# Performance work log

Hardware: AMD Instinct MI355X
Metric: run time of the kernel (lower is better)

## Reference

```python
import jax, jax.numpy as jnp
import numpy as np

N_TP = 4  # number of heterogeneous agent types (experts)


def _mlp(x, w1, b1, w2, b2, w3, b3):
    h = jax.nn.relu(x @ w1 + b1)
    h = jax.nn.relu(h @ w2 + b2)
    return h @ w3 + b3


def setup_inputs() -> dict:
    key = jax.random.key(0)
    ks = jax.random.split(key, 12)
    T, A, D, H, NA = 2048, 128, 64, 64, 16
    s = 0.05
    return {
        "obs": jax.random.normal(ks[0], (T, A, D), dtype=jnp.float32),
        "hete_pick": jax.random.randint(ks[1], (T, A), 0, N_TP, dtype=jnp.int64),
        "gp_sel_summary": jax.random.uniform(ks[2], (T, N_TP), dtype=jnp.float32),
        "W1": jax.random.normal(ks[3], (N_TP, D + N_TP, H), dtype=jnp.float32) * s,
        "b1": jnp.zeros((N_TP, H), jnp.float32),
        "W2": jax.random.normal(ks[4], (N_TP, H, H), dtype=jnp.float32) * s,
        "b2": jnp.zeros((N_TP, H), jnp.float32),
        "W3": jax.random.normal(ks[5], (N_TP, H, NA), dtype=jnp.float32) * s,
        "b3": jnp.zeros((N_TP, NA), jnp.float32),
        "cW1": jax.random.normal(ks[6], (D + N_TP, H), dtype=jnp.float32) * s,
        "cb1": jnp.zeros((H,), jnp.float32),
        "cW2": jax.random.normal(ks[7], (H, H), dtype=jnp.float32) * s,
        "cb2": jnp.zeros((H,), jnp.float32),
        "cW3": jax.random.normal(ks[8], (H, 1), dtype=jnp.float32) * s,
        "cb3": jnp.zeros((1,), jnp.float32),
    }


def reference(obs, hete_pick, gp_sel_summary, W1, b1, W2, b2, W3, b3,
              cW1, cb1, cW2, cb2, cW3, cb3):
    T, A, D = obs.shape
    n_tp = W1.shape[0]
    # hete_info_obs: broadcast group-selection summary over agents, concat to obs
    hete_info = jnp.broadcast_to(gp_sel_summary[:, None, :], (T, A, n_tp))
    x = jnp.concatenate([obs, hete_info.astype(obs.dtype)], axis=-1)  # [T,A,D+n_tp]
    xf = x.reshape(T * A, D + n_tp)
    tp = hete_pick.reshape(T * A)
    # per-type dispatch: mask -> sub-net -> scatter back (expressed as masked select)
    logits = jnp.zeros((T * A, W3.shape[-1]), obs.dtype)
    for t in range(n_tp):
        out_t = _mlp(xf, W1[t], b1[t], W2[t], b2[t], W3[t], b3[t])
        logits = jnp.where((tp == t)[:, None], out_t, logits)
    # central critic runs on all agents
    value = _mlp(xf, cW1, cb1, cW2, cb2, cW3, cb3)  # [T*A,1]
    out = jnp.concatenate([logits, value], axis=-1)  # [T*A, n_action+1]
    return out.reshape(T, A, -1)
```

## Files before the change

kernel.cpp:

```cpp
#include <hip/hip_runtime.h>
#include <stdint.h>


typedef float v4f __attribute__((ext_vector_type(4)));
typedef short v8s __attribute__((ext_vector_type(8)));

#define XS_STR 104
#define HS_STR 136
#define WP2_OFF 30720
#define WP3_OFF 51200

static __device__ __forceinline__ short f2bf(float f) {
    union { float f; uint32_t u; } c; c.f = f;
    uint32_t u = c.u;
    uint32_t r = (u + 0x7FFFu + ((u >> 16) & 1u)) >> 16;
    return (short)r;
}


__global__ void count_kernel(const int* __restrict__ hete, int* __restrict__ cnt) {
    __shared__ int wc[4][4];
    int tid = threadIdx.x, lane = tid & 63, w = tid >> 6;
    int base = blockIdx.x * 1024;
    int lc[4] = {0, 0, 0, 0};
#pragma unroll
    for (int c = 0; c < 4; c++) {
        int e = hete[base + c * 256 + tid];
#pragma unroll
        for (int t = 0; t < 4; t++) {
            unsigned long long m = __ballot(e == t);
            if (lane == 0) lc[t] += __popcll(m);
        }
    }
    if (lane == 0)
#pragma unroll
        for (int t = 0; t < 4; t++) wc[w][t] = lc[t];
    __syncthreads();
    if (tid < 4)
        cnt[blockIdx.x * 4 + tid] = wc[0][tid] + wc[1][tid] + wc[2][tid] + wc[3][tid];
}

__global__ void prefix_kernel(const int* __restrict__ cnt, int* __restrict__ hdr,
                              int* __restrict__ bb, int* __restrict__ bucket) {
    __shared__ int s[4][256];
    __shared__ int sa[5], sC[4];
    int tid = threadIdx.x;
    int c0[4];
#pragma unroll
    for (int t = 0; t < 4; t++) { c0[t] = cnt[tid * 4 + t]; s[t][tid] = c0[t]; }
    __syncthreads();
    for (int off = 1; off < 256; off <<= 1) {
        int v[4];
#pragma unroll
        for (int t = 0; t < 4; t++) v[t] = (tid >= off) ? s[t][tid - off] : 0;
        __syncthreads();
#pragma unroll
        for (int t = 0; t < 4; t++) s[t][tid] += v[t];
        __syncthreads();
    }
    if (tid == 0) {
        int a = 0, ts = 0;
        for (int e = 0; e < 4; e++) {
            int c = s[e][255];
            sC[e] = c;
            sa[e] = a;
            hdr[8 + e]  = a;
            hdr[13 + e] = ts;
            int tiles = (c + 127) >> 7;
            a  += tiles << 7;
            ts += tiles;
        }
        sa[4]   = a;
        hdr[12] = a;
        hdr[17] = ts;
    }
    __syncthreads();
#pragma unroll
    for (int t = 0; t < 4; t++) bb[tid * 4 + t] = sa[t] + s[t][tid] - c0[t];
    for (int e = 0; e < 4; e++) {
        int start = sa[e] + sC[e], end = sa[e + 1];
        for (int i = start + tid; i < end; i += 256) bucket[i] = -1;
    }
}

__global__ void scatter_kernel(const int* __restrict__ hete, const int* __restrict__ bb,
                               int* __restrict__ bucket) {
    __shared__ int cur[4];
    int tid = threadIdx.x, lane = tid & 63;
    if (tid < 4) cur[tid] = bb[blockIdx.x * 4 + tid];
    __syncthreads();
    unsigned long long lt = (1ull << lane) - 1ull;
#pragma unroll
    for (int c = 0; c < 4; c++) {
        int i = blockIdx.x * 1024 + c * 256 + tid;
        int e = hete[i];
        int slot = 0;
#pragma unroll
        for (int t = 0; t < 4; t++) {
            unsigned long long m = __ballot(e == t);
            int n = __popcll(m);
            int wb = 0;
            if (lane == 0 && n) wb = atomicAdd(&cur[t], n);
            wb = __shfl(wb, 0);
            if (e == t) slot = wb + __popcll(m & lt);
        }
        bucket[slot] = i;
    }
}

__global__ void prep_kernel(const float* __restrict__ W1, const float* __restrict__ cW1,
                            const float* __restrict__ W2, const float* __restrict__ cW2,
                            const float* __restrict__ W3, const float* __restrict__ cW3,
                            short* __restrict__ wp) {
    int b = blockIdx.x, lane = threadIdx.x;
    int nl = lane & 15, quad = lane >> 4;
    short frag[8];
    if (b < 60) {
        int e = b / 12, rem = b % 12, ks = rem / 4, nt = rem % 4;
        int n = nt * 16 + nl;
#pragma unroll
        for (int j = 0; j < 8; j++) {
            int k = ks * 32 + quad * 8 + j;
            float v = 0.f;
            if (k < 68) v = (e < 4) ? W1[(e * 68 + k) * 64 + n] : cW1[k * 64 + n];
            frag[j] = f2bf(v);
        }
    } else if (b < 100) {
        int u = b - 60, e = u / 8, ks = (u % 8) / 4, nt = u % 4;
        int n = nt * 16 + nl;
#pragma unroll
        for (int j = 0; j < 8; j++) {
            int k = ks * 32 + quad * 8 + j;
            frag[j] = f2bf((e < 4) ? W2[(e * 64 + k) * 64 + n] : cW2[k * 64 + n]);
        }
    } else {
        int u = b - 100;
#pragma unroll
        for (int j = 0; j < 8; j++) {
            int ks = (u < 8) ? (u & 1) : (u - 8);
            int k  = ks * 32 + quad * 8 + j;
            float v;
            if (u < 8) { int ee = u >> 1; v = W3[(ee * 64 + k) * 16 + nl]; }
            else       { v = (nl == 0) ? cW3[k] : 0.f; }
            frag[j] = f2bf(v);
        }
    }
    v8s pk = { frag[0], frag[1], frag[2], frag[3], frag[4], frag[5], frag[6], frag[7] };
    *(v8s*)(wp + (size_t)b * 512 + lane * 8) = pk;
}


__global__ __launch_bounds__(256) void main_kernel(
    const float* __restrict__ obs, const float* __restrict__ gp,
    const int* __restrict__ bucket, const int* __restrict__ hdr,
    const short* __restrict__ wp,
    const float* __restrict__ b1, const float* __restrict__ b2, const float* __restrict__ b3,
    const float* __restrict__ cb1, const float* __restrict__ cb2, const float* __restrict__ cb3,
    float* __restrict__ out)
{
    __shared__ __align__(16) short buf[128 * HS_STR];
    __shared__ int tokL[128];
    short* xs = buf;
    short* hs = buf;

    int b = blockIdx.x;
    int total = hdr[17];
    if (b >= total) return;
    int e = 3;
    if      (b < hdr[14]) e = 0;
    else if (b < hdr[15]) e = 1;
    else if (b < hdr[16]) e = 2;
    int slot0 = hdr[8 + e] + (b - hdr[13 + e]) * 128;

    int tid = threadIdx.x, lane = tid & 63, w = tid >> 6;
    int ml = lane & 15, quad = lane >> 4;

    if (tid < 128) tokL[tid] = bucket[slot0 + tid];

    {
        int r = tid >> 1, hh = tid & 1;
        int tk = bucket[slot0 + r];
        v8s z = { 0, 0, 0, 0, 0, 0, 0, 0 };
        if (tk >= 0) {
            const float4* src = (const float4*)(obs + (size_t)tk * 64 + hh * 32);
#pragma unroll
            for (int t = 0; t < 4; t++) {
                float4 f0 = src[2 * t], f1 = src[2 * t + 1];
                v8s pk = { f2bf(f0.x), f2bf(f0.y), f2bf(f0.z), f2bf(f0.w),
                           f2bf(f1.x), f2bf(f1.y), f2bf(f1.z), f2bf(f1.w) };
                *(v8s*)&xs[r * XS_STR + hh * 32 + t * 8] = pk;
            }
            if (hh) {
                const float* g = gp + (size_t)(tk >> 7) * 4;
                v8s pg = { f2bf(g[0]), f2bf(g[1]), f2bf(g[2]), f2bf(g[3]), 0, 0, 0, 0 };
                *(v8s*)&xs[r * XS_STR + 64] = pg;
                *(v8s*)&xs[r * XS_STR + 72] = z;
                *(v8s*)&xs[r * XS_STR + 80] = z;
                *(v8s*)&xs[r * XS_STR + 88] = z;
            }
        } else {
#pragma unroll
            for (int t = 0; t < 4; t++) *(v8s*)&xs[r * XS_STR + hh * 32 + t * 8] = z;
            if (hh) {
                *(v8s*)&xs[r * XS_STR + 64] = z;
                *(v8s*)&xs[r * XS_STR + 72] = z;
                *(v8s*)&xs[r * XS_STR + 80] = z;
                *(v8s*)&xs[r * XS_STR + 88] = z;
            }
        }
    }
    __syncthreads();

    v4f accE[8], accC[8];
#pragma unroll
    for (int m = 0; m < 8; m++) { accE[m] = (v4f){0,0,0,0}; accC[m] = (v4f){0,0,0,0}; }
#pragma unroll
    for (int ks = 0; ks < 3; ks++) {
        v8s bE = *(const v8s*)(wp + (size_t)((e * 3 + ks) * 4 + w) * 512 + lane * 8);
        v8s bC = *(const v8s*)(wp + (size_t)((12 + ks) * 4 + w) * 512 + lane * 8);
#pragma unroll
        for (int m = 0; m < 8; m++) {
            v8s a = *(const v8s*)&xs[(m * 16 + ml) * XS_STR + ks * 32 + quad * 8];
            accE[m] = __builtin_amdgcn_mfma_f32_16x16x32_bf16(a, bE, accE[m], 0, 0, 0);
            accC[m] = __builtin_amdgcn_mfma_f32_16x16x32_bf16(a, bC, accC[m], 0, 0, 0);
        }
    }
    __syncthreads();
    {
        float bE1 = b1[e * 64 + w * 16 + ml], bC1 = cb1[w * 16 + ml];
#pragma unroll
        for (int m = 0; m < 8; m++)
#pragma unroll
            for (int rr = 0; rr < 4; rr++) {
                int row = m * 16 + quad * 4 + rr;
                hs[row * HS_STR + w * 16 + ml]      = f2bf(fmaxf(accE[m][rr] + bE1, 0.f));
                hs[row * HS_STR + 64 + w * 16 + ml] = f2bf(fmaxf(accC[m][rr] + bC1, 0.f));
            }
    }
    __syncthreads();

    v4f acc2E[8], acc2C[8];
#pragma unroll
    for (int m = 0; m < 8; m++) { acc2E[m] = (v4f){0,0,0,0}; acc2C[m] = (v4f){0,0,0,0}; }
#pragma unroll
    for (int ks = 0; ks < 2; ks++) {
        v8s bE = *(const v8s*)(wp + WP2_OFF + (size_t)((e * 2 + ks) * 4 + w) * 512 + lane * 8);
        v8s bC = *(const v8s*)(wp + WP2_OFF + (size_t)((8 + ks) * 4 + w) * 512 + lane * 8);
#pragma unroll
        for (int m = 0; m < 8; m++) {
            v8s aE = *(const v8s*)&hs[(m * 16 + ml) * HS_STR + ks * 32 + quad * 8];
            v8s aC = *(const v8s*)&hs[(m * 16 + ml) * HS_STR + 64 + ks * 32 + quad * 8];
            acc2E[m] = __builtin_amdgcn_mfma_f32_16x16x32_bf16(aE, bE, acc2E[m], 0, 0, 0);
            acc2C[m] = __builtin_amdgcn_mfma_f32_16x16x32_bf16(aC, bC, acc2C[m], 0, 0, 0);
        }
    }
    __syncthreads();
    {
        float bE2 = b2[e * 64 + w * 16 + ml], bC2 = cb2[w * 16 + ml];
#pragma unroll
        for (int m = 0; m < 8; m++)
#pragma unroll
            for (int rr = 0; rr < 4; rr++) {
                int row = m * 16 + quad * 4 + rr;
                hs[row * HS_STR + w * 16 + ml]      = f2bf(fmaxf(acc2E[m][rr] + bE2, 0.f));
                hs[row * HS_STR + 64 + w * 16 + ml] = f2bf(fmaxf(acc2C[m][rr] + bC2, 0.f));
            }
    }
    __syncthreads();

    v4f accL[2], accV[2];
#pragma unroll
    for (int mm = 0; mm < 2; mm++) { accL[mm] = (v4f){0,0,0,0}; accV[mm] = (v4f){0,0,0,0}; }
#pragma unroll
    for (int ks = 0; ks < 2; ks++) {
        v8s bW = *(const v8s*)(wp + WP3_OFF + (size_t)(e * 2 + ks) * 512 + lane * 8);
        v8s bV = *(const v8s*)(wp + WP3_OFF + (size_t)(8 + ks) * 512 + lane * 8);
#pragma unroll
        for (int mm = 0; mm < 2; mm++) {
            v8s aE = *(const v8s*)&hs[((2 * w + mm) * 16 + ml) * HS_STR + ks * 32 + quad * 8];
            v8s aC = *(const v8s*)&hs[((2 * w + mm) * 16 + ml) * HS_STR + 64 + ks * 32 + quad * 8];
            accL[mm] = __builtin_amdgcn_mfma_f32_16x16x32_bf16(aE, bW, accL[mm], 0, 0, 0);
            accV[mm] = __builtin_amdgcn_mfma_f32_16x16x32_bf16(aC, bV, accV[mm], 0, 0, 0);
        }
    }

    {
        float b3v = b3[e * 16 + ml], cb3v = cb3[0];
#pragma unroll
        for (int mm = 0; mm < 2; mm++)
#pragma unroll
            for (int rr = 0; rr < 4; rr++) {
                int row = (2 * w + mm) * 16 + quad * 4 + rr;
                int tk = tokL[row];
                if (tk >= 0) {
                    float* o = out + (size_t)tk * 17;
                    o[ml] = accL[mm][rr] + b3v;
                    if (ml == 0) o[16] = accV[mm][rr] + cb3v;
                }
            }
    }
}


extern "C" void kernel_launch(void* const* d_in, const int* in_sizes, int n_in,
                              void* d_out, int out_size, void* d_ws, size_t ws_size,
                              hipStream_t stream) {
    const float* obs = (const float*)d_in[0];
    const int*  hete = (const int*)d_in[1];
    const float* gp  = (const float*)d_in[2];
    const float* W1  = (const float*)d_in[3];
    const float* b1  = (const float*)d_in[4];
    const float* W2  = (const float*)d_in[5];
    const float* b2  = (const float*)d_in[6];
    const float* W3  = (const float*)d_in[7];
    const float* b3  = (const float*)d_in[8];
    const float* cW1 = (const float*)d_in[9];
    const float* cb1 = (const float*)d_in[10];
    const float* cW2 = (const float*)d_in[11];
    const float* cb2 = (const float*)d_in[12];
    const float* cW3 = (const float*)d_in[13];
    const float* cb3 = (const float*)d_in[14];
    float* out = (float*)d_out;

    int*   hdr    = (int*)d_ws;
    int*   bucket = hdr + 32;
    int*   cnt    = bucket + 262656;
    int*   bb     = cnt + 1024;
    short* wp     = (short*)(bb + 1024);

    count_kernel  <<<256, 256, 0, stream>>>(hete, cnt);
    prefix_kernel <<<1,   256, 0, stream>>>(cnt, hdr, bb, bucket);
    scatter_kernel<<<256, 256, 0, stream>>>(hete, bb, bucket);
    prep_kernel   <<<110,  64, 0, stream>>>(W1, cW1, W2, cW2, W3, cW3, wp);
    main_kernel   <<<2051, 256, 0, stream>>>(obs, gp, bucket, hdr, wp,
                                             b1, b2, b3, cb1, cb2, cb3, out);
}
```

Baseline: 157.8 us.

## Replace global bucket sort with per-block local expert grouping

Removes the count, prefix and scatter kernels and instead has each block take 128 contiguous tokens, sort them by expert type in shared memory via ballots, and pad each expert group to 16-row tiles (up to 11 tiles). Per-tile expert weights are selected through a packed expert map. This drops three kernel launches and the gathered obs reads through a global bucket array, at the cost of padding waste (up to 176 rows instead of 128), per-tile weight loads, and larger register and shared-memory use. It also adds launch_bounds occupancy hint 3.

```diff
diff --git a/kernel.cpp b/kernel.cpp
--- a/kernel.cpp
+++ b/kernel.cpp
@@ -7,105 +7,19 @@
 
 #define XS_STR 104
 #define HS_STR 136
+#define MAXR   176
+#define MAXT   11
 #define WP2_OFF 30720
 #define WP3_OFF 51200
+
+#define SEL4(te, a0, a1, a2, a3) \
+    ((te) < 2 ? ((te) == 0 ? (a0) : (a1)) : ((te) == 2 ? (a2) : (a3)))
 
 static __device__ __forceinline__ short f2bf(float f) {
     union { float f; uint32_t u; } c; c.f = f;
     uint32_t u = c.u;
     uint32_t r = (u + 0x7FFFu + ((u >> 16) & 1u)) >> 16;
     return (short)r;
-}
-
-
-__global__ void count_kernel(const int* __restrict__ hete, int* __restrict__ cnt) {
-    __shared__ int wc[4][4];
-    int tid = threadIdx.x, lane = tid & 63, w = tid >> 6;
-    int base = blockIdx.x * 1024;
-    int lc[4] = {0, 0, 0, 0};
-#pragma unroll
-    for (int c = 0; c < 4; c++) {
-        int e = hete[base + c * 256 + tid];
-#pragma unroll
-        for (int t = 0; t < 4; t++) {
-            unsigned long long m = __ballot(e == t);
-            if (lane == 0) lc[t] += __popcll(m);
-        }
-    }
-    if (lane == 0)
-#pragma unroll
-        for (int t = 0; t < 4; t++) wc[w][t] = lc[t];
-    __syncthreads();
-    if (tid < 4)
-        cnt[blockIdx.x * 4 + tid] = wc[0][tid] + wc[1][tid] + wc[2][tid] + wc[3][tid];
-}
-
-__global__ void prefix_kernel(const int* __restrict__ cnt, int* __restrict__ hdr,
-                              int* __restrict__ bb, int* __restrict__ bucket) {
-    __shared__ int s[4][256];
-    __shared__ int sa[5], sC[4];
-    int tid = threadIdx.x;
-    int c0[4];
-#pragma unroll
-    for (int t = 0; t < 4; t++) { c0[t] = cnt[tid * 4 + t]; s[t][tid] = c0[t]; }
-    __syncthreads();
-    for (int off = 1; off < 256; off <<= 1) {
-        int v[4];
-#pragma unroll
-        for (int t = 0; t < 4; t++) v[t] = (tid >= off) ? s[t][tid - off] : 0;
-        __syncthreads();
-#pragma unroll
-        for (int t = 0; t < 4; t++) s[t][tid] += v[t];
-        __syncthreads();
-    }
-    if (tid == 0) {
-        int a = 0, ts = 0;
-        for (int e = 0; e < 4; e++) {
-            int c = s[e][255];
-            sC[e] = c;
-            sa[e] = a;
-            hdr[8 + e]  = a;
-            hdr[13 + e] = ts;
-            int tiles = (c + 127) >> 7;
-            a  += tiles << 7;
-            ts += tiles;
-        }
-        sa[4]   = a;
-        hdr[12] = a;
-        hdr[17] = ts;
-    }
-    __syncthreads();
-#pragma unroll
-    for (int t = 0; t < 4; t++) bb[tid * 4 + t] = sa[t] + s[t][tid] - c0[t];
-    for (int e = 0; e < 4; e++) {
-        int start = sa[e] + sC[e], end = sa[e + 1];
-        for (int i = start + tid; i < end; i += 256) bucket[i] = -1;
-    }
-}
-
-__global__ void scatter_kernel(const int* __restrict__ hete, const int* __restrict__ bb,
-                               int* __restrict__ bucket) {
-    __shared__ int cur[4];
-    int tid = threadIdx.x, lane = tid & 63;
-    if (tid < 4) cur[tid] = bb[blockIdx.x * 4 + tid];
-    __syncthreads();
-    unsigned long long lt = (1ull << lane) - 1ull;
-#pragma unroll
-    for (int c = 0; c < 4; c++) {
-        int i = blockIdx.x * 1024 + c * 256 + tid;
-        int e = hete[i];
-        int slot = 0;
-#pragma unroll
-        for (int t = 0; t < 4; t++) {
-            unsigned long long m = __ballot(e == t);
-            int n = __popcll(m);
-            int wb = 0;
-            if (lane == 0 && n) wb = atomicAdd(&cur[t], n);
-            wb = __shfl(wb, 0);
-            if (e == t) slot = wb + __popcll(m & lt);
-        }
-        bucket[slot] = i;
-    }
 }
 
 __global__ void prep_kernel(const float* __restrict__ W1, const float* __restrict__ cW1,
@@ -150,154 +64,245 @@
 }
 
 
-__global__ __launch_bounds__(256) void main_kernel(
-    const float* __restrict__ obs, const float* __restrict__ gp,
-    const int* __restrict__ bucket, const int* __restrict__ hdr,
-    const short* __restrict__ wp,
+__global__ __launch_bounds__(256, 3) void main_kernel(
+    const float* __restrict__ obs, const int* __restrict__ hete,
+    const float* __restrict__ gp, const short* __restrict__ wp,
     const float* __restrict__ b1, const float* __restrict__ b2, const float* __restrict__ b3,
     const float* __restrict__ cb1, const float* __restrict__ cb2, const float* __restrict__ cb3,
     float* __restrict__ out)
 {
-    __shared__ __align__(16) short buf[128 * HS_STR];
-    __shared__ int tokL[128];
+    __shared__ __align__(16) short buf[MAXR * HS_STR];
+    __shared__ int rowtok[MAXR];
+    __shared__ int tslot[128];
+    __shared__ int wcnt[2][4];
+
     short* xs = buf;
     short* hs = buf;
 
-    int b = blockIdx.x;
-    int total = hdr[17];
-    if (b >= total) return;
-    int e = 3;
-    if      (b < hdr[14]) e = 0;
-    else if (b < hdr[15]) e = 1;
-    else if (b < hdr[16]) e = 2;
-    int slot0 = hdr[8 + e] + (b - hdr[13 + e]) * 128;
-
-    int tid = threadIdx.x, lane = tid & 63, w = tid >> 6;
-    int ml = lane & 15, quad = lane >> 4;
-
-    if (tid < 128) tokL[tid] = bucket[slot0 + tid];
+    const int b = blockIdx.x;
+    const int tid = threadIdx.x, lane = tid & 63, w = tid >> 6;
+    const int ml = lane & 15, quad = lane >> 4;
+    const int col = w * 16 + ml;
+    const size_t base = (size_t)b * 128;
+
+    const int ltk = tid >> 1, hh = tid & 1;
+    const float4* src = (const float4*)(obs + (base + ltk) * 64 + hh * 32);
+    float4 f[8];
+#pragma unroll
+    for (int t = 0; t < 8; t++) f[t] = src[t];
+
+    const float* gpb = gp + (size_t)b * 4;
+    float g0 = gpb[0], g1 = gpb[1], g2 = gpb[2], g3 = gpb[3];
+
+    if (tid < MAXR) rowtok[tid] = -1;
+
+    int e = 0, rank = 0;
+    if (tid < 128) {
+        e = hete[base + tid];
+        unsigned long long ltm = (1ull << lane) - 1ull;
+        unsigned long long m0 = __ballot(e == 0);
+        unsigned long long m1 = __ballot(e == 1);
+        unsigned long long m2 = __ballot(e == 2);
+        unsigned long long m3 = __ballot(e == 3);
+        if      (e == 0) rank = __popcll(m0 & ltm);
+        else if (e == 1) rank = __popcll(m1 & ltm);
+        else if (e == 2) rank = __popcll(m2 & ltm);
+        else             rank = __popcll(m3 & ltm);
+        if (lane == 0) {
+            wcnt[w][0] = __popcll(m0); wcnt[w][1] = __popcll(m1);
+            wcnt[w][2] = __popcll(m2); wcnt[w][3] = __popcll(m3);
+        }
+    }
+    __syncthreads();
+
+    int c0 = wcnt[0][0] + wcnt[1][0];
+    int c1 = wcnt[0][1] + wcnt[1][1];
+    int c2 = wcnt[0][2] + wcnt[1][2];
+    int c3 = wcnt[0][3] + wcnt[1][3];
+    int p0 = (c0 + 15) & ~15, p1 = (c1 + 15) & ~15;
+    int p2 = (c2 + 15) & ~15, p3 = (c3 + 15) & ~15;
+    int gs1 = p0, gs2 = p0 + p1, gs3 = p0 + p1 + p2;
+    int padded = gs3 + p3;
+    int ntiles = padded >> 4;
+    int n1 = p1 >> 4, n2 = p2 >> 4, n3 = p3 >> 4;
+    int t1 = gs1 >> 4, t2 = gs2 >> 4, t3 = gs3 >> 4;
+    int epack = ((0x55555555 & ((1 << (2 * n1)) - 1)) * 1) << (2 * t1)
+              | ((0x55555555 & ((1 << (2 * n2)) - 1)) * 2) << (2 * t2)
+              | ((0x55555555 & ((1 << (2 * n3)) - 1)) * 3) << (2 * t3);
+
+    if (tid < 128) {
+        int gsE  = SEL4(e, 0, gs1, gs2, gs3);
+        int woff = (w == 1) ? wcnt[0][e] : 0;
+        int slot = gsE + woff + rank;
+        rowtok[slot] = tid;
+        tslot[tid]   = slot;
+    }
+    __syncthreads();
 
     {
-        int r = tid >> 1, hh = tid & 1;
-        int tk = bucket[slot0 + r];
         v8s z = { 0, 0, 0, 0, 0, 0, 0, 0 };
-        if (tk >= 0) {
-            const float4* src = (const float4*)(obs + (size_t)tk * 64 + hh * 32);
-#pragma unroll
-            for (int t = 0; t < 4; t++) {
-                float4 f0 = src[2 * t], f1 = src[2 * t + 1];
-                v8s pk = { f2bf(f0.x), f2bf(f0.y), f2bf(f0.z), f2bf(f0.w),
-                           f2bf(f1.x), f2bf(f1.y), f2bf(f1.z), f2bf(f1.w) };
-                *(v8s*)&xs[r * XS_STR + hh * 32 + t * 8] = pk;
-            }
-            if (hh) {
-                const float* g = gp + (size_t)(tk >> 7) * 4;
-                v8s pg = { f2bf(g[0]), f2bf(g[1]), f2bf(g[2]), f2bf(g[3]), 0, 0, 0, 0 };
-                *(v8s*)&xs[r * XS_STR + 64] = pg;
-                *(v8s*)&xs[r * XS_STR + 72] = z;
-                *(v8s*)&xs[r * XS_STR + 80] = z;
-                *(v8s*)&xs[r * XS_STR + 88] = z;
-            }
-        } else {
-#pragma unroll
-            for (int t = 0; t < 4; t++) *(v8s*)&xs[r * XS_STR + hh * 32 + t * 8] = z;
-            if (hh) {
-                *(v8s*)&xs[r * XS_STR + 64] = z;
-                *(v8s*)&xs[r * XS_STR + 72] = z;
-                *(v8s*)&xs[r * XS_STR + 80] = z;
-                *(v8s*)&xs[r * XS_STR + 88] = z;
-            }
-        }
-    }
-    __syncthreads();
-
-    v4f accE[8], accC[8];
-#pragma unroll
-    for (int m = 0; m < 8; m++) { accE[m] = (v4f){0,0,0,0}; accC[m] = (v4f){0,0,0,0}; }
+        int s = tslot[ltk];
+        int rb = s * XS_STR + hh * 32;
+#pragma unroll
+        for (int t = 0; t < 4; t++) {
+            float4 a0 = f[2 * t], a1 = f[2 * t + 1];
+            v8s pk = { f2bf(a0.x), f2bf(a0.y), f2bf(a0.z), f2bf(a0.w),
+                       f2bf(a1.x), f2bf(a1.y), f2bf(a1.z), f2bf(a1.w) };
+            *(v8s*)&xs[rb + t * 8] = pk;
+        }
+        if (hh) {
+            v8s pg = { f2bf(g0), f2bf(g1), f2bf(g2), f2bf(g3), 0, 0, 0, 0 };
+            *(v8s*)&xs[s * XS_STR + 64] = pg;
+            *(v8s*)&xs[s * XS_STR + 72] = z;
+            *(v8s*)&xs[s * XS_STR + 80] = z;
+            *(v8s*)&xs[s * XS_STR + 88] = z;
+        }
+#pragma unroll
+        for (int p = 0; p < 2; p++) {
+            int r = p * 128 + ltk;
+            if (r < padded && rowtok[r] < 0) {
+#pragma unroll
+                for (int t = 0; t < 4; t++) *(v8s*)&xs[r * XS_STR + hh * 32 + t * 8] = z;
+                if (hh) {
+                    *(v8s*)&xs[r * XS_STR + 64] = z;
+                    *(v8s*)&xs[r * XS_STR + 72] = z;
+                    *(v8s*)&xs[r * XS_STR + 80] = z;
+                    *(v8s*)&xs[r * XS_STR + 88] = z;
+                }
+            }
+        }
+    }
+    __syncthreads();
+
+    v4f accE[MAXT], accC[MAXT];
+#pragma unroll
+    for (int mt = 0; mt < MAXT; mt++) { accE[mt] = (v4f){0,0,0,0}; accC[mt] = (v4f){0,0,0,0}; }
+
+    v8s bC1f[3];
+#pragma unroll
+    for (int ks = 0; ks < 3; ks++)
+        bC1f[ks] = *(const v8s*)(wp + (size_t)((12 + ks) * 4 + w) * 512 + lane * 8);
+
 #pragma unroll
     for (int ks = 0; ks < 3; ks++) {
-        v8s bE = *(const v8s*)(wp + (size_t)((e * 3 + ks) * 4 + w) * 512 + lane * 8);
-        v8s bC = *(const v8s*)(wp + (size_t)((12 + ks) * 4 + w) * 512 + lane * 8);
-#pragma unroll
-        for (int m = 0; m < 8; m++) {
-            v8s a = *(const v8s*)&xs[(m * 16 + ml) * XS_STR + ks * 32 + quad * 8];
-            accE[m] = __builtin_amdgcn_mfma_f32_16x16x32_bf16(a, bE, accE[m], 0, 0, 0);
-            accC[m] = __builtin_amdgcn_mfma_f32_16x16x32_bf16(a, bC, accC[m], 0, 0, 0);
-        }
-    }
-    __syncthreads();
+#pragma unroll
+        for (int mt = 0; mt < MAXT; mt++) {
+            if (mt < ntiles) {
+                int te = (epack >> (2 * mt)) & 3;
+                v8s bE = *(const v8s*)(wp + (size_t)((te * 3 + ks) * 4 + w) * 512 + lane * 8);
+                v8s a  = *(const v8s*)&xs[(mt * 16 + ml) * XS_STR + ks * 32 + quad * 8];
+                accE[mt] = __builtin_amdgcn_mfma_f32_16x16x32_bf16(a, bE,       accE[mt], 0, 0, 0);
+                accC[mt] = __builtin_amdgcn_mfma_f32_16x16x32_bf16(a, bC1f[ks], accC[mt], 0, 0, 0);
+            }
+        }
+    }
+    __syncthreads();
+
     {
-        float bE1 = b1[e * 64 + w * 16 + ml], bC1 = cb1[w * 16 + ml];
-#pragma unroll
-        for (int m = 0; m < 8; m++)
-#pragma unroll
-            for (int rr = 0; rr < 4; rr++) {
-                int row = m * 16 + quad * 4 + rr;
-                hs[row * HS_STR + w * 16 + ml]      = f2bf(fmaxf(accE[m][rr] + bE1, 0.f));
-                hs[row * HS_STR + 64 + w * 16 + ml] = f2bf(fmaxf(accC[m][rr] + bC1, 0.f));
-            }
-    }
-    __syncthreads();
-
-    v4f acc2E[8], acc2C[8];
-#pragma unroll
-    for (int m = 0; m < 8; m++) { acc2E[m] = (v4f){0,0,0,0}; acc2C[m] = (v4f){0,0,0,0}; }
+        float b1e0 = b1[col], b1e1 = b1[64 + col], b1e2 = b1[128 + col], b1e3 = b1[192 + col];
+        float cb1v = cb1[col];
+#pragma unroll
+        for (int mt = 0; mt < MAXT; mt++) {
+            if (mt < ntiles) {
+                int te = (epack >> (2 * mt)) & 3;
+                float bv = SEL4(te, b1e0, b1e1, b1e2, b1e3);
+#pragma unroll
+                for (int rr = 0; rr < 4; rr++) {
+                    int row = mt * 16 + quad * 4 + rr;
+                    hs[row * HS_STR + col]      = f2bf(fmaxf(accE[mt][rr] + bv,   0.f));
+                    hs[row * HS_STR + 64 + col] = f2bf(fmaxf(accC[mt][rr] + cb1v, 0.f));
+                }
+            }
+        }
+    }
+    __syncthreads();
+
+    v4f acc2E[MAXT], acc2C[MAXT];
+#pragma unroll
+    for (int mt = 0; mt < MAXT; mt++) { acc2E[mt] = (v4f){0,0,0,0}; acc2C[mt] = (v4f){0,0,0,0}; }
+
+    v8s bC2f[2];
+#pragma unroll
+    for (int ks = 0; ks < 2; ks++)
+        bC2f[ks] = *(const v8s*)(wp + WP2_OFF + (size_t)((8 + ks) * 4 + w) * 512 + lane * 8);
+
 #pragma unroll
     for (int ks = 0; ks < 2; ks++) {
-        v8s bE = *(const v8s*)(wp + WP2_OFF + (size_t)((e * 2 + ks) * 4 + w) * 512 + lane * 8);
-        v8s bC = *(const v8s*)(wp + WP2_OFF + (size_t)((8 + ks) * 4 + w) * 512 + lane * 8);
-#pragma unroll
-        for (int m = 0; m < 8; m++) {
-            v8s aE = *(const v8s*)&hs[(m * 16 + ml) * HS_STR + ks * 32 + quad * 8];
-            v8s aC = *(const v8s*)&hs[(m * 16 + ml) * HS_STR + 64 + ks * 32 + quad * 8];
-            acc2E[m] = __builtin_amdgcn_mfma_f32_16x16x32_bf16(aE, bE, acc2E[m], 0, 0, 0);
-            acc2C[m] = __builtin_amdgcn_mfma_f32_16x16x32_bf16(aC, bC, acc2C[m], 0, 0, 0);
-        }
-    }
-    __syncthreads();
+#pragma unroll
+        for (int mt = 0; mt < MAXT; mt++) {
+            if (mt < ntiles) {
+                int te = (epack >> (2 * mt)) & 3;
+                v8s bE = *(const v8s*)(wp + WP2_OFF + (size_t)((te * 2 + ks) * 4 + w) * 512 + lane * 8);
+                v8s aE = *(const v8s*)&hs[(mt * 16 + ml) * HS_STR + ks * 32 + quad * 8];
+                v8s aC = *(const v8s*)&hs[(mt * 16 + ml) * HS_STR + 64 + ks * 32 + quad * 8];
+                acc2E[mt] = __builtin_amdgcn_mfma_f32_16x16x32_bf16(aE, bE,       acc2E[mt], 0, 0, 0);
+                acc2C[mt] = __builtin_amdgcn_mfma_f32_16x16x32_bf16(aC, bC2f[ks], acc2C[mt], 0, 0, 0);
+            }
+        }
+    }
+    __syncthreads();
+
     {
-        float bE2 = b2[e * 64 + w * 16 + ml], bC2 = cb2[w * 16 + ml];
-#pragma unroll
-        for (int m = 0; m < 8; m++)
-#pragma unroll
-            for (int rr = 0; rr < 4; rr++) {
-                int row = m * 16 + quad * 4 + rr;
-                hs[row * HS_STR + w * 16 + ml]      = f2bf(fmaxf(acc2E[m][rr] + bE2, 0.f));
-                hs[row * HS_STR + 64 + w * 16 + ml] = f2bf(fmaxf(acc2C[m][rr] + bC2, 0.f));
-            }
-    }
-    __syncthreads();
-
-    v4f accL[2], accV[2];
-#pragma unroll
-    for (int mm = 0; mm < 2; mm++) { accL[mm] = (v4f){0,0,0,0}; accV[mm] = (v4f){0,0,0,0}; }
+        float b2e0 = b2[col], b2e1 = b2[64 + col], b2e2 = b2[128 + col], b2e3 = b2[192 + col];
+        float cb2v = cb2[col];
+#pragma unroll
+        for (int mt = 0; mt < MAXT; mt++) {
+            if (mt < ntiles) {
+                int te = (epack >> (2 * mt)) & 3;
+                float bv = SEL4(te, b2e0, b2e1, b2e2, b2e3);
+#pragma unroll
+                for (int rr = 0; rr < 4; rr++) {
+                    int row = mt * 16 + quad * 4 + rr;
+                    hs[row * HS_STR + col]      = f2bf(fmaxf(acc2E[mt][rr] + bv,   0.f));
+                    hs[row * HS_STR + 64 + col] = f2bf(fmaxf(acc2C[mt][rr] + cb2v, 0.f));
+                }
+            }
+        }
+    }
+    __syncthreads();
+
+    v4f accL[3], accV[3];
+#pragma unroll
+    for (int j = 0; j < 3; j++) { accL[j] = (v4f){0,0,0,0}; accV[j] = (v4f){0,0,0,0}; }
+
 #pragma unroll
     for (int ks = 0; ks < 2; ks++) {
-        v8s bW = *(const v8s*)(wp + WP3_OFF + (size_t)(e * 2 + ks) * 512 + lane * 8);
         v8s bV = *(const v8s*)(wp + WP3_OFF + (size_t)(8 + ks) * 512 + lane * 8);
 #pragma unroll
-        for (int mm = 0; mm < 2; mm++) {
-            v8s aE = *(const v8s*)&hs[((2 * w + mm) * 16 + ml) * HS_STR + ks * 32 + quad * 8];
-            v8s aC = *(const v8s*)&hs[((2 * w + mm) * 16 + ml) * HS_STR + 64 + ks * 32 + quad * 8];
-            accL[mm] = __builtin_amdgcn_mfma_f32_16x16x32_bf16(aE, bW, accL[mm], 0, 0, 0);
-            accV[mm] = __builtin_amdgcn_mfma_f32_16x16x32_bf16(aC, bV, accV[mm], 0, 0, 0);
+        for (int j = 0; j < 3; j++) {
+            int mt = w + 4 * j;
+            if (mt < ntiles) {
+                int te = (epack >> (2 * mt)) & 3;
+                v8s bW = *(const v8s*)(wp + WP3_OFF + (size_t)(te * 2 + ks) * 512 + lane * 8);
+                v8s aE = *(const v8s*)&hs[(mt * 16 + ml) * HS_STR + ks * 32 + quad * 8];
+                v8s aC = *(const v8s*)&hs[(mt * 16 + ml) * HS_STR + 64 + ks * 32 + quad * 8];
+                accL[j] = __builtin_amdgcn_mfma_f32_16x16x32_bf16(aE, bW, accL[j], 0, 0, 0);
+                accV[j] = __builtin_amdgcn_mfma_f32_16x16x32_bf16(aC, bV, accV[j], 0, 0, 0);
+            }
         }
     }
 
     {
-        float b3v = b3[e * 16 + ml], cb3v = cb3[0];
-#pragma unroll
-        for (int mm = 0; mm < 2; mm++)
-#pragma unroll
-            for (int rr = 0; rr < 4; rr++) {
-                int row = (2 * w + mm) * 16 + quad * 4 + rr;
-                int tk = tokL[row];
-                if (tk >= 0) {
-                    float* o = out + (size_t)tk * 17;
-                    o[ml] = accL[mm][rr] + b3v;
-                    if (ml == 0) o[16] = accV[mm][rr] + cb3v;
+        float b3e0 = b3[ml], b3e1 = b3[16 + ml], b3e2 = b3[32 + ml], b3e3 = b3[48 + ml];
+        float cb3v = cb3[0];
+#pragma unroll
+        for (int j = 0; j < 3; j++) {
+            int mt = w + 4 * j;
+            if (mt < ntiles) {
+                int te = (epack >> (2 * mt)) & 3;
+                float bv = SEL4(te, b3e0, b3e1, b3e2, b3e3);
+#pragma unroll
+                for (int rr = 0; rr < 4; rr++) {
+                    int r = mt * 16 + quad * 4 + rr;
+                    int tk = rowtok[r];
+                    if (tk >= 0) {
+                        float* o = out + (base + tk) * 17;
+                        o[ml] = accL[j][rr] + bv;
+                        if (ml == 0) o[16] = accV[j][rr] + cb3v;
+                    }
                 }
             }
+        }
     }
 }
 
@@ -322,16 +327,9 @@
     const float* cb3 = (const float*)d_in[14];
     float* out = (float*)d_out;
 
-    int*   hdr    = (int*)d_ws;
-    int*   bucket = hdr + 32;
-    int*   cnt    = bucket + 262656;
-    int*   bb     = cnt + 1024;
-    short* wp     = (short*)(bb + 1024);
-
-    count_kernel  <<<256, 256, 0, stream>>>(hete, cnt);
-    prefix_kernel <<<1,   256, 0, stream>>>(cnt, hdr, bb, bucket);
-    scatter_kernel<<<256, 256, 0, stream>>>(hete, bb, bucket);
-    prep_kernel   <<<110,  64, 0, stream>>>(W1, cW1, W2, cW2, W3, cW3, wp);
-    main_kernel   <<<2051, 256, 0, stream>>>(obs, gp, bucket, hdr, wp,
-                                             b1, b2, b3, cb1, cb2, cb3, out);
+    short* wp = (short*)d_ws;
+
+    prep_kernel<<<110,  64, 0, stream>>>(W1, cW1, W2, cW2, W3, cW3, wp);
+    main_kernel<<<2048, 256, 0, stream>>>(obs, hete, gp, wp,
+                                          b1, b2, b3, cb1, cb2, cb3, out);
 }
```

After: 165.4 us. +4.8%, slower.

## Keep MLP activations in registers with transposed MFMA chaining and folded biases

Applied to the files above, without the earlier changes.

The main kernel now computes each layer as weights × tokens, so an MFMA output fragment can be reused directly as the next layer's B operand. This removes the shared-memory staging of inputs and hidden states and the block barriers between layers. Biases b1 and b2 are folded into the packed weight fragments through a constant-one input column, and prep_kernel permutes the K ordering to match the accumulator layout. The expert's weights are copied into LDS once per block, while critic weights are read straight from global memory. The packed weight buffer is moved to alias the count scratch region, which makes correctness depend on the exact fragment permutation and on the workspace layout.

```diff
diff --git a/kernel.cpp b/kernel.cpp
--- a/kernel.cpp
+++ b/kernel.cpp
@@ -4,17 +4,14 @@
 
 typedef float v4f __attribute__((ext_vector_type(4)));
 typedef short v8s __attribute__((ext_vector_type(8)));
-
-#define XS_STR 104
-#define HS_STR 136
-#define WP2_OFF 30720
-#define WP3_OFF 51200
+typedef float v4fa __attribute__((ext_vector_type(4), aligned(4)));
+
+#define MFMA __builtin_amdgcn_mfma_f32_16x16x32_bf16
 
 static __device__ __forceinline__ short f2bf(float f) {
-    union { float f; uint32_t u; } c; c.f = f;
-    uint32_t u = c.u;
-    uint32_t r = (u + 0x7FFFu + ((u >> 16) & 1u)) >> 16;
-    return (short)r;
+    union { __bf16 b; short s; } u;
+    u.b = (__bf16)f;
+    return u.s;
 }
 
 
@@ -111,6 +108,8 @@
 __global__ void prep_kernel(const float* __restrict__ W1, const float* __restrict__ cW1,
                             const float* __restrict__ W2, const float* __restrict__ cW2,
                             const float* __restrict__ W3, const float* __restrict__ cW3,
+                            const float* __restrict__ b1, const float* __restrict__ cb1,
+                            const float* __restrict__ b2, const float* __restrict__ cb2,
                             short* __restrict__ wp) {
     int b = blockIdx.x, lane = threadIdx.x;
     int nl = lane & 15, quad = lane >> 4;
@@ -122,26 +121,36 @@
         for (int j = 0; j < 8; j++) {
             int k = ks * 32 + quad * 8 + j;
             float v = 0.f;
-            if (k < 68) v = (e < 4) ? W1[(e * 68 + k) * 64 + n] : cW1[k * 64 + n];
+            if (k < 68)       v = (e < 4) ? W1[(e * 68 + k) * 64 + n] : cW1[k * 64 + n];
+            else if (k == 68) v = (e < 4) ? b1[e * 64 + n] : cb1[n];
             frag[j] = f2bf(v);
         }
     } else if (b < 100) {
-        int u = b - 60, e = u / 8, ks = (u % 8) / 4, nt = u % 4;
-        int n = nt * 16 + nl;
+        int u = b - 60, net = u / 8, ks = (u & 7) >> 2, m = u & 3;
+        int n = m * 16 + nl;
 #pragma unroll
         for (int j = 0; j < 8; j++) {
-            int k = ks * 32 + quad * 8 + j;
-            frag[j] = f2bf((e < 4) ? W2[(e * 64 + k) * 64 + n] : cW2[k * 64 + n]);
-        }
-    } else {
+            int kin = ks * 32 + 16 * (j >> 2) + quad * 4 + (j & 3);
+            frag[j] = f2bf((net < 4) ? W2[(net * 64 + kin) * 64 + n] : cW2[kin * 64 + n]);
+        }
+    } else if (b < 110) {
         int u = b - 100;
 #pragma unroll
         for (int j = 0; j < 8; j++) {
             int ks = (u < 8) ? (u & 1) : (u - 8);
-            int k  = ks * 32 + quad * 8 + j;
+            int kin = ks * 32 + 16 * (j >> 2) + quad * 4 + (j & 3);
             float v;
-            if (u < 8) { int ee = u >> 1; v = W3[(ee * 64 + k) * 16 + nl]; }
-            else       { v = (nl == 0) ? cW3[k] : 0.f; }
+            if (u < 8) { int net = u >> 1; v = W3[(net * 64 + kin) * 16 + nl]; }
+            else       { v = (nl == 0) ? cW3[kin] : 0.f; }
+            frag[j] = f2bf(v);
+        }
+    } else {
+        int u = b - 110, net = u / 4, m = u % 4;
+        int n = m * 16 + nl;
+#pragma unroll
+        for (int j = 0; j < 8; j++) {
+            float v = 0.f;
+            if (quad == 0 && j == 0) v = (net < 4) ? b2[net * 64 + n] : cb2[n];
             frag[j] = f2bf(v);
         }
     }
@@ -150,155 +159,235 @@
 }
 
 
-__global__ __launch_bounds__(256) void main_kernel(
+__global__ __launch_bounds__(256, 4) void main_kernel(
     const float* __restrict__ obs, const float* __restrict__ gp,
     const int* __restrict__ bucket, const int* __restrict__ hdr,
     const short* __restrict__ wp,
-    const float* __restrict__ b1, const float* __restrict__ b2, const float* __restrict__ b3,
-    const float* __restrict__ cb1, const float* __restrict__ cb2, const float* __restrict__ cb3,
+    const float* __restrict__ b3, const float* __restrict__ cb3,
     float* __restrict__ out)
 {
-    __shared__ __align__(16) short buf[128 * HS_STR];
-    __shared__ int tokL[128];
-    short* xs = buf;
-    short* hs = buf;
-
-    int b = blockIdx.x;
-    int total = hdr[17];
+    __shared__ __align__(16) short lwp[26 * 512];
+
+    const int b = blockIdx.x;
+    const int total = hdr[17];
     if (b >= total) return;
     int e = 3;
     if      (b < hdr[14]) e = 0;
     else if (b < hdr[15]) e = 1;
     else if (b < hdr[16]) e = 2;
-    int slot0 = hdr[8 + e] + (b - hdr[13 + e]) * 128;
-
-    int tid = threadIdx.x, lane = tid & 63, w = tid >> 6;
-    int ml = lane & 15, quad = lane >> 4;
-
-    if (tid < 128) tokL[tid] = bucket[slot0 + tid];
+    const int slot0 = hdr[8 + e] + (b - hdr[13 + e]) * 128;
+
+    const int tid = threadIdx.x, lane = tid & 63, w = tid >> 6;
+    const int nl = lane & 15, quad = lane >> 4;
 
     {
-        int r = tid >> 1, hh = tid & 1;
-        int tk = bucket[slot0 + r];
+        const uint4* wp4 = (const uint4*)wp;
+        uint4* l4 = (uint4*)lwp;
+        for (int i = tid; i < 26 * 64; i += 256) {
+            int lb = i >> 6, off = i & 63;
+            int g = (lb < 12) ? (e * 12 + lb)
+                  : (lb < 20) ? (60 + e * 8 + lb - 12)
+                  : (lb < 24) ? (110 + e * 4 + lb - 20)
+                              : (100 + e * 2 + lb - 24);
+            l4[i] = wp4[(size_t)g * 64 + off];
+        }
+    }
+
+    const int tk0 = bucket[slot0 + w * 32 + nl];
+    const int tk1 = bucket[slot0 + w * 32 + 16 + nl];
+
+    v8s xb0[2], xb1[2], gf0, gf1;
+    {
         v8s z = { 0, 0, 0, 0, 0, 0, 0, 0 };
-        if (tk >= 0) {
-            const float4* src = (const float4*)(obs + (size_t)tk * 64 + hh * 32);
-#pragma unroll
-            for (int t = 0; t < 4; t++) {
-                float4 f0 = src[2 * t], f1 = src[2 * t + 1];
-                v8s pk = { f2bf(f0.x), f2bf(f0.y), f2bf(f0.z), f2bf(f0.w),
-                           f2bf(f1.x), f2bf(f1.y), f2bf(f1.z), f2bf(f1.w) };
-                *(v8s*)&xs[r * XS_STR + hh * 32 + t * 8] = pk;
-            }
-            if (hh) {
-                const float* g = gp + (size_t)(tk >> 7) * 4;
-                v8s pg = { f2bf(g[0]), f2bf(g[1]), f2bf(g[2]), f2bf(g[3]), 0, 0, 0, 0 };
-                *(v8s*)&xs[r * XS_STR + 64] = pg;
-                *(v8s*)&xs[r * XS_STR + 72] = z;
-                *(v8s*)&xs[r * XS_STR + 80] = z;
-                *(v8s*)&xs[r * XS_STR + 88] = z;
-            }
-        } else {
-#pragma unroll
-            for (int t = 0; t < 4; t++) *(v8s*)&xs[r * XS_STR + hh * 32 + t * 8] = z;
-            if (hh) {
-                *(v8s*)&xs[r * XS_STR + 64] = z;
-                *(v8s*)&xs[r * XS_STR + 72] = z;
-                *(v8s*)&xs[r * XS_STR + 80] = z;
-                *(v8s*)&xs[r * XS_STR + 88] = z;
-            }
-        }
-    }
+        xb0[0] = xb0[1] = xb1[0] = xb1[1] = gf0 = gf1 = z;
+        if (tk0 >= 0) {
+#pragma unroll
+            for (int ks = 0; ks < 2; ks++) {
+                const float4* s = (const float4*)(obs + (size_t)tk0 * 64 + ks * 32 + quad * 8);
+                float4 a = s[0], c = s[1];
+                xb0[ks] = (v8s){ f2bf(a.x), f2bf(a.y), f2bf(a.z), f2bf(a.w),
+                                 f2bf(c.x), f2bf(c.y), f2bf(c.z), f2bf(c.w) };
+            }
+            if (quad == 0) {
+                float4 g = *(const float4*)(gp + (size_t)(tk0 >> 7) * 4);
+                gf0 = (v8s){ f2bf(g.x), f2bf(g.y), f2bf(g.z), f2bf(g.w),
+                             (short)0x3F80, 0, 0, 0 };
+            }
+        }
+        if (tk1 >= 0) {
+#pragma unroll
+            for (int ks = 0; ks < 2; ks++) {
+                const float4* s = (const float4*)(obs + (size_t)tk1 * 64 + ks * 32 + quad * 8);
+                float4 a = s[0], c = s[1];
+                xb1[ks] = (v8s){ f2bf(a.x), f2bf(a.y), f2bf(a.z), f2bf(a.w),
+                                 f2bf(c.x), f2bf(c.y), f2bf(c.z), f2bf(c.w) };
+            }
+            if (quad == 0) {
+                float4 g = *(const float4*)(gp + (size_t)(tk1 >> 7) * 4);
+                gf1 = (v8s){ f2bf(g.x), f2bf(g.y), f2bf(g.z), f2bf(g.w),
+                             (short)0x3F80, 0, 0, 0 };
+            }
+        }
+    }
+    v8s onef = (v8s){ 0, 0, 0, 0, 0, 0, 0, 0 };
+    if (quad == 0) onef[0] = (short)0x3F80;
+
     __syncthreads();
 
-    v4f accE[8], accC[8];
-#pragma unroll
-    for (int m = 0; m < 8; m++) { accE[m] = (v4f){0,0,0,0}; accC[m] = (v4f){0,0,0,0}; }
-#pragma unroll
-    for (int ks = 0; ks < 3; ks++) {
-        v8s bE = *(const v8s*)(wp + (size_t)((e * 3 + ks) * 4 + w) * 512 + lane * 8);
-        v8s bC = *(const v8s*)(wp + (size_t)((12 + ks) * 4 + w) * 512 + lane * 8);
-#pragma unroll
-        for (int m = 0; m < 8; m++) {
-            v8s a = *(const v8s*)&xs[(m * 16 + ml) * XS_STR + ks * 32 + quad * 8];
-            accE[m] = __builtin_amdgcn_mfma_f32_16x16x32_bf16(a, bE, accE[m], 0, 0, 0);
-            accC[m] = __builtin_amdgcn_mfma_f32_16x16x32_bf16(a, bC, accC[m], 0, 0, 0);
-        }
-    }
-    __syncthreads();
+#define LFRAG(lb) (*(const v8s*)&lwp[(size_t)(lb) * 512 + lane * 8])
+#define WFRAG(g)  (*(const v8s*)(wp + (size_t)(g) * 512 + lane * 8))
+
     {
-        float bE1 = b1[e * 64 + w * 16 + ml], bC1 = cb1[w * 16 + ml];
-#pragma unroll
-        for (int m = 0; m < 8; m++)
-#pragma unroll
-            for (int rr = 0; rr < 4; rr++) {
-                int row = m * 16 + quad * 4 + rr;
-                hs[row * HS_STR + w * 16 + ml]      = f2bf(fmaxf(accE[m][rr] + bE1, 0.f));
-                hs[row * HS_STR + 64 + w * 16 + ml] = f2bf(fmaxf(accC[m][rr] + bC1, 0.f));
-            }
-    }
-    __syncthreads();
-
-    v4f acc2E[8], acc2C[8];
-#pragma unroll
-    for (int m = 0; m < 8; m++) { acc2E[m] = (v4f){0,0,0,0}; acc2C[m] = (v4f){0,0,0,0}; }
-#pragma unroll
-    for (int ks = 0; ks < 2; ks++) {
-        v8s bE = *(const v8s*)(wp + WP2_OFF + (size_t)((e * 2 + ks) * 4 + w) * 512 + lane * 8);
-        v8s bC = *(const v8s*)(wp + WP2_OFF + (size_t)((8 + ks) * 4 + w) * 512 + lane * 8);
-#pragma unroll
-        for (int m = 0; m < 8; m++) {
-            v8s aE = *(const v8s*)&hs[(m * 16 + ml) * HS_STR + ks * 32 + quad * 8];
-            v8s aC = *(const v8s*)&hs[(m * 16 + ml) * HS_STR + 64 + ks * 32 + quad * 8];
-            acc2E[m] = __builtin_amdgcn_mfma_f32_16x16x32_bf16(aE, bE, acc2E[m], 0, 0, 0);
-            acc2C[m] = __builtin_amdgcn_mfma_f32_16x16x32_bf16(aC, bC, acc2C[m], 0, 0, 0);
-        }
-    }
-    __syncthreads();
+        v4f aA[4], aB[4];
+#pragma unroll
+        for (int m = 0; m < 4; m++) {
+            v8s wg = LFRAG(8 + m);
+            aA[m] = MFMA(wg, gf0, (v4f){0, 0, 0, 0}, 0, 0, 0);
+            aB[m] = MFMA(wg, gf1, (v4f){0, 0, 0, 0}, 0, 0, 0);
+        }
+#pragma unroll
+        for (int ks = 0; ks < 2; ks++)
+#pragma unroll
+            for (int m = 0; m < 4; m++) {
+                v8s wk = LFRAG(ks * 4 + m);
+                aA[m] = MFMA(wk, xb0[ks], aA[m], 0, 0, 0);
+                aB[m] = MFMA(wk, xb1[ks], aB[m], 0, 0, 0);
+            }
+
+        v8s pA[2], pB[2];
+#pragma unroll
+        for (int ks = 0; ks < 2; ks++) {
+            v8s ta, tb;
+#pragma unroll
+            for (int j = 0; j < 8; j++) {
+                ta[j] = f2bf(fmaxf(aA[2 * ks + (j >> 2)][j & 3], 0.f));
+                tb[j] = f2bf(fmaxf(aB[2 * ks + (j >> 2)][j & 3], 0.f));
+            }
+            pA[ks] = ta; pB[ks] = tb;
+        }
+
+        v4f cA[4], cB[4];
+#pragma unroll
+        for (int m = 0; m < 4; m++) {
+            v8s bf = LFRAG(20 + m);
+            cA[m] = MFMA(bf, onef, (v4f){0, 0, 0, 0}, 0, 0, 0);
+            cB[m] = MFMA(bf, onef, (v4f){0, 0, 0, 0}, 0, 0, 0);
+        }
+#pragma unroll
+        for (int ks = 0; ks < 2; ks++)
+#pragma unroll
+            for (int m = 0; m < 4; m++) {
+                v8s wk = LFRAG(12 + ks * 4 + m);
+                cA[m] = MFMA(wk, pA[ks], cA[m], 0, 0, 0);
+                cB[m] = MFMA(wk, pB[ks], cB[m], 0, 0, 0);
+            }
+
+        v8s qA[2], qB[2];
+#pragma unroll
+        for (int ks = 0; ks < 2; ks++) {
+            v8s ta, tb;
+#pragma unroll
+            for (int j = 0; j < 8; j++) {
+                ta[j] = f2bf(fmaxf(cA[2 * ks + (j >> 2)][j & 3], 0.f));
+                tb[j] = f2bf(fmaxf(cB[2 * ks + (j >> 2)][j & 3], 0.f));
+            }
+            qA[ks] = ta; qB[ks] = tb;
+        }
+
+        v4f LA = (v4f){0, 0, 0, 0}, LB = (v4f){0, 0, 0, 0};
+#pragma unroll
+        for (int ks = 0; ks < 2; ks++) {
+            v8s wk = LFRAG(24 + ks);
+            LA = MFMA(wk, qA[ks], LA, 0, 0, 0);
+            LB = MFMA(wk, qB[ks], LB, 0, 0, 0);
+        }
+
+        v4fa b3v = *(const v4fa*)(b3 + e * 16 + quad * 4);
+        if (tk0 >= 0) {
+            float* o = out + (size_t)tk0 * 17;
+            v4fa ov = { LA[0] + b3v[0], LA[1] + b3v[1], LA[2] + b3v[2], LA[3] + b3v[3] };
+            *(v4fa*)(o + quad * 4) = ov;
+        }
+        if (tk1 >= 0) {
+            float* o = out + (size_t)tk1 * 17;
+            v4fa ov = { LB[0] + b3v[0], LB[1] + b3v[1], LB[2] + b3v[2], LB[3] + b3v[3] };
+            *(v4fa*)(o + quad * 4) = ov;
+        }
+    }
+
     {
-        float bE2 = b2[e * 64 + w * 16 + ml], bC2 = cb2[w * 16 + ml];
-#pragma unroll
-        for (int m = 0; m < 8; m++)
-#pragma unroll
-            for (int rr = 0; rr < 4; rr++) {
-                int row = m * 16 + quad * 4 + rr;
-                hs[row * HS_STR + w * 16 + ml]      = f2bf(fmaxf(acc2E[m][rr] + bE2, 0.f));
-                hs[row * HS_STR + 64 + w * 16 + ml] = f2bf(fmaxf(acc2C[m][rr] + bC2, 0.f));
-            }
-    }
-    __syncthreads();
-
-    v4f accL[2], accV[2];
-#pragma unroll
-    for (int mm = 0; mm < 2; mm++) { accL[mm] = (v4f){0,0,0,0}; accV[mm] = (v4f){0,0,0,0}; }
-#pragma unroll
-    for (int ks = 0; ks < 2; ks++) {
-        v8s bW = *(const v8s*)(wp + WP3_OFF + (size_t)(e * 2 + ks) * 512 + lane * 8);
-        v8s bV = *(const v8s*)(wp + WP3_OFF + (size_t)(8 + ks) * 512 + lane * 8);
-#pragma unroll
-        for (int mm = 0; mm < 2; mm++) {
-            v8s aE = *(const v8s*)&hs[((2 * w + mm) * 16 + ml) * HS_STR + ks * 32 + quad * 8];
-            v8s aC = *(const v8s*)&hs[((2 * w + mm) * 16 + ml) * HS_STR + 64 + ks * 32 + quad * 8];
-            accL[mm] = __builtin_amdgcn_mfma_f32_16x16x32_bf16(aE, bW, accL[mm], 0, 0, 0);
-            accV[mm] = __builtin_amdgcn_mfma_f32_16x16x32_bf16(aC, bV, accV[mm], 0, 0, 0);
-        }
-    }
-
-    {
-        float b3v = b3[e * 16 + ml], cb3v = cb3[0];
-#pragma unroll
-        for (int mm = 0; mm < 2; mm++)
-#pragma unroll
-            for (int rr = 0; rr < 4; rr++) {
-                int row = (2 * w + mm) * 16 + quad * 4 + rr;
-                int tk = tokL[row];
-                if (tk >= 0) {
-                    float* o = out + (size_t)tk * 17;
-                    o[ml] = accL[mm][rr] + b3v;
-                    if (ml == 0) o[16] = accV[mm][rr] + cb3v;
-                }
-            }
-    }
+        v4f aA[4], aB[4];
+#pragma unroll
+        for (int m = 0; m < 4; m++) {
+            v8s wg = WFRAG(56 + m);
+            aA[m] = MFMA(wg, gf0, (v4f){0, 0, 0, 0}, 0, 0, 0);
+            aB[m] = MFMA(wg, gf1, (v4f){0, 0, 0, 0}, 0, 0, 0);
+        }
+#pragma unroll
+        for (int ks = 0; ks < 2; ks++)
+#pragma unroll
+            for (int m = 0; m < 4; m++) {
+                v8s wk = WFRAG(48 + ks * 4 + m);
+                aA[m] = MFMA(wk, xb0[ks], aA[m], 0, 0, 0);
+                aB[m] = MFMA(wk, xb1[ks], aB[m], 0, 0, 0);
+            }
+
+        v8s pA[2], pB[2];
+#pragma unroll
+        for (int ks = 0; ks < 2; ks++) {
+            v8s ta, tb;
+#pragma unroll
+            for (int j = 0; j < 8; j++) {
+                ta[j] = f2bf(fmaxf(aA[2 * ks + (j >> 2)][j & 3], 0.f));
+                tb[j] = f2bf(fmaxf(aB[2 * ks + (j >> 2)][j & 3], 0.f));
+            }
+            pA[ks] = ta; pB[ks] = tb;
+        }
+
+        v4f cA[4], cB[4];
+#pragma unroll
+        for (int m = 0; m < 4; m++) {
+            v8s bf = WFRAG(126 + m);
+            cA[m] = MFMA(bf, onef, (v4f){0, 0, 0, 0}, 0, 0, 0);
+            cB[m] = MFMA(bf, onef, (v4f){0, 0, 0, 0}, 0, 0, 0);
+        }
+#pragma unroll
+        for (int ks = 0; ks < 2; ks++)
+#pragma unroll
+            for (int m = 0; m < 4; m++) {
+                v8s wk = WFRAG(92 + ks * 4 + m);
+                cA[m] = MFMA(wk, pA[ks], cA[m], 0, 0, 0);
+                cB[m] = MFMA(wk, pB[ks], cB[m], 0, 0, 0);
+            }
+
+        v8s qA[2], qB[2];
+#pragma unroll
+        for (int ks = 0; ks < 2; ks++) {
+            v8s ta, tb;
+#pragma unroll
+            for (int j = 0; j < 8; j++) {
+                ta[j] = f2bf(fmaxf(cA[2 * ks + (j >> 2)][j & 3], 0.f));
+                tb[j] = f2bf(fmaxf(cB[2 * ks + (j >> 2)][j & 3], 0.f));
+            }
+            qA[ks] = ta; qB[ks] = tb;
+        }
+
+        v4f VA = (v4f){0, 0, 0, 0}, VB = (v4f){0, 0, 0, 0};
+#pragma unroll
+        for (int ks = 0; ks < 2; ks++) {
+            v8s wk = WFRAG(108 + ks);
+            VA = MFMA(wk, qA[ks], VA, 0, 0, 0);
+            VB = MFMA(wk, qB[ks], VB, 0, 0, 0);
+        }
+
+        if (quad == 0) {
+            float cb3v = cb3[0];
+            if (tk0 >= 0) out[(size_t)tk0 * 17 + 16] = VA[0] + cb3v;
+            if (tk1 >= 0) out[(size_t)tk1 * 17 + 16] = VB[0] + cb3v;
+        }
+    }
+#undef LFRAG
+#undef WFRAG
 }
 
 
@@ -326,12 +415,13 @@
     int*   bucket = hdr + 32;
     int*   cnt    = bucket + 262656;
     int*   bb     = cnt + 1024;
-    short* wp     = (short*)(bb + 1024);
+    short* wp     = (short*)cnt;
 
     count_kernel  <<<256, 256, 0, stream>>>(hete, cnt);
     prefix_kernel <<<1,   256, 0, stream>>>(cnt, hdr, bb, bucket);
     scatter_kernel<<<256, 256, 0, stream>>>(hete, bb, bucket);
-    prep_kernel   <<<110,  64, 0, stream>>>(W1, cW1, W2, cW2, W3, cW3, wp);
+    prep_kernel   <<<130,  64, 0, stream>>>(W1, cW1, W2, cW2, W3, cW3,
+                                            b1, cb1, b2, cb2, wp);
     main_kernel   <<<2051, 256, 0, stream>>>(obs, gp, bucket, hdr, wp,
-                                             b1, b2, b3, cb1, cb2, cb3, out);
-}
+                                             b3, cb3, out);
+}
```

New measurement: 156.7 us. Within noise of the previous version (-0.7%).
